# Kernel optimization log

Measured on AMD Instinct MI355X. Metric: run time of the kernel, lower is better.

## Reference

```python
import jax, jax.numpy as jnp
import numpy as np

N, F, T, C, E = 5000, 4, 12, 600, 160000


def setup_inputs() -> dict:
    key = jax.random.key(0)
    ks = jax.random.split(key, 18)
    x = jax.random.normal(ks[0], (N, F, T), jnp.float32)
    edge_index = jax.random.randint(ks[1], (2, E), 0, N)
    edge_attributes = jax.random.uniform(ks[2], (E,), jnp.float32)
    s_in = 0.5   # glorot-ish scale for F->C conv weights
    s_lin = 0.03  # scale for (2C)->C gate linears
    return {
        "x": x,
        "edge_index": edge_index,
        "edge_attributes": edge_attributes,
        # GCNConv weights/biases for z, r, h gates (weight stored [F, C])
        "W_z": jax.random.normal(ks[3], (F, C), jnp.float32) * s_in,
        "b_z": jnp.zeros((C,), jnp.float32),
        "W_r": jax.random.normal(ks[4], (F, C), jnp.float32) * s_in,
        "b_r": jnp.zeros((C,), jnp.float32),
        "W_h": jax.random.normal(ks[5], (F, C), jnp.float32) * s_in,
        "b_h": jnp.zeros((C,), jnp.float32),
        # gate Linear(2C, C) weights in torch layout [out=C, in=2C]
        "Wlz": jax.random.normal(ks[6], (C, 2 * C), jnp.float32) * s_lin,
        "blz": jnp.zeros((C,), jnp.float32),
        "Wlr": jax.random.normal(ks[7], (C, 2 * C), jnp.float32) * s_lin,
        "blr": jnp.zeros((C,), jnp.float32),
        "Wlh": jax.random.normal(ks[8], (C, 2 * C), jnp.float32) * s_lin,
        "blh": jnp.zeros((C,), jnp.float32),
        # temporal attention logits over periods
        "att": jax.random.normal(ks[9], (T,), jnp.float32),
        # head Linear(600, periods), torch layout [T, C]
        "W_head": jax.random.normal(ks[10], (T, C), jnp.float32) * 0.04,
        "b_head": jnp.zeros((T,), jnp.float32),
    }


def _gcn_propagate(x, edge_index, edge_weight):
    """A_hat @ x with A_hat = D^{-1/2}(A+I)D^{-1/2} (GCNConv norm, self-loops w=1).
    x: [N, F, T] -> [N, F, T]."""
    loop = jnp.arange(N)
    row = jnp.concatenate([edge_index[0], loop])   # source j
    col = jnp.concatenate([edge_index[1], loop])   # target i
    w = jnp.concatenate([edge_weight, jnp.ones((N,), x.dtype)])
    deg = jax.ops.segment_sum(w, col, num_segments=N)
    dis = jnp.where(deg > 0, jax.lax.rsqrt(deg), 0.0)
    norm = dis[row] * w * dis[col]                 # [E+N]
    msgs = norm[:, None, None] * x[row]            # gather + scale, [E+N, F, T]
    return jax.ops.segment_sum(msgs, col, num_segments=N)


def reference(x, edge_index, edge_attributes,
              W_z, b_z, W_r, b_r, W_h, b_h,
              Wlz, blz, Wlr, blr, Wlh, blh,
              att, W_head, b_head):
    # A3TGCN: H is passed as None each period -> zeros, never threaded across
    # time. Hence z*H == 0 and the H*r candidate term == 0 exactly; the r-gate
    # (W_r, b_r, Wlr, blr) and the second halves of Wlz/Wlh drop out of the math.
    agg = _gcn_propagate(x, edge_index, edge_attributes)          # [N, F, T]
    # GCNConv output = A_hat X W + b (linear commutes with propagation)
    conv_z = jnp.einsum('nft,fc->nct', agg, W_z) + b_z[:, None]   # [N, C, T]
    conv_h = jnp.einsum('nft,fc->nct', agg, W_h) + b_h[:, None]
    # gate linears on cat([conv, H]) with H = 0 -> only first C input columns
    z = jax.nn.sigmoid(jnp.einsum('nct,dc->ndt', conv_z, Wlz[:, :C]) + blz[:, None])
    h_tilde = jnp.tanh(jnp.einsum('nct,dc->ndt', conv_h, Wlh[:, :C]) + blh[:, None])
    H_t = (1.0 - z) * h_tilde                                      # z*H = 0
    probs = jax.nn.softmax(att)                                    # [T]
    H_accum = jnp.einsum('nct,t->nc', H_t, probs)                  # [N, C]
    return jax.nn.relu(H_accum) @ W_head.T + b_head                # [N, T]
```

## Files before the change

### kernel.cpp

```cpp
#include <hip/hip_runtime.h>

#define NN 5000
#define NF 4
#define NT 12
#define NC 600
#define NCP 640
#define NE 160000
#define FT 48
#define LOG2E 1.4426950408889634f

typedef float v2f __attribute__((ext_vector_type(2)));


__global__ void k_init(float* __restrict__ degcnt, float* __restrict__ tabG) {
    int i = blockIdx.x * blockDim.x + threadIdx.x;
    if (i < 10000) degcnt[i] = 0.f;
    else if (i < 24092) tabG[i - 10000] = 0.f;
}

#define CNT_BLOCKS 625
#define WB_WAVES 6132
__global__ __launch_bounds__(256) void k_count(
        const int* __restrict__ ei, const float* __restrict__ w,
        int* __restrict__ cnt, float* __restrict__ deg, int* __restrict__ rank,
        const float* __restrict__ Wz, const float* __restrict__ bz,
        const float* __restrict__ Wh, const float* __restrict__ bh,
        const float* __restrict__ Wlz, const float* __restrict__ blz,
        const float* __restrict__ Wlh, const float* __restrict__ blh,
        const float* __restrict__ att, const float* __restrict__ Whead,
        float* __restrict__ tabG) {
    int bid = blockIdx.x;
    int tid = threadIdx.x;
    if (bid < CNT_BLOCKS) {
        int e = bid * 256 + tid;
        if (e < NE) {
            int c = ei[NE + e];
            rank[e] = atomicAdd(&cnt[c], 1);
            atomicAdd(&deg[c], w[e]);
        }
        return;
    }
    int wid = (bid - CNT_BLOCKS) * 4 + (tid >> 6);
    int lane = tid & 63;
    if (wid >= WB_WAVES) return;

    if (wid < 6000) {
        const float* va;
        const float* vb;
        float scale, bias = 0.f;
        if (wid < 2400) {
            int f = wid / NC, d = wid % NC;
            va = Wz + f * NC; vb = Wlz + d * (2 * NC); scale = LOG2E;
        } else if (wid < 4800) {
            int j = wid - 2400;
            int f = j / NC, d = j % NC;
            va = Wh + f * NC; vb = Wlh + d * (2 * NC); scale = 2.0f * LOG2E;
        } else if (wid < 5400) {
            int d = wid - 4800;
            va = bz; vb = Wlz + d * (2 * NC); scale = LOG2E; bias = blz[d];
        } else {
            int d = wid - 5400;
            va = bh; vb = Wlh + d * (2 * NC); scale = 2.0f * LOG2E; bias = blh[d];
        }
        float s = 0.f;
        for (int c = lane; c < NC; c += 64) s = fmaf(va[c], vb[c], s);
#pragma unroll
        for (int off = 32; off > 0; off >>= 1) s += __shfl_down(s, off, 64);
        if (lane == 0) {
            float r = scale * (bias + s);
            if (wid < 2400) {
                int f = wid / NC, d = wid % NC;
                tabG[d * 4 + f] = r;
            } else if (wid < 4800) {
                int j = wid - 2400;
                int f = j / NC, d = j % NC;
                tabG[2560 + d * 4 + f] = r;
            } else if (wid < 5400) {
                tabG[5120 + (wid - 4800) * 2] = r;
            } else {
                tabG[5120 + (wid - 5400) * 2 + 1] = r;
            }
        }
    } else if (wid < 6012) {
        if (lane == 0) {
            int t = wid - 6000;
            float m = att[0];
            for (int k = 1; k < NT; ++k) m = fmaxf(m, att[k]);
            float ssum = 0.f;
            for (int k = 0; k < NT; ++k) ssum += __expf(att[k] - m);
            tabG[14080 + t] = __expf(att[t] - m) / ssum;
        }
    } else {
        int i = (wid - 6012) * 64 + lane;
        if (i < 7680) {
            int j = i & 3;
            int rest = i >> 2;
            int d = rest % NCP, q = rest / NCP;
            float v = (d < NC) ? Whead[(4 * q + j) * NC + d] : 0.f;
            tabG[6400 + i] = v;
        }
    }
}

#define SCAN_CHUNK 20
__global__ __launch_bounds__(256) void k_scan(const int* __restrict__ cnt,
                                              const float* __restrict__ deg,
                                              int* __restrict__ base,
                                              float* __restrict__ dis) {
    __shared__ int part[256];
    int t = threadIdx.x;
    int start = t * SCAN_CHUNK;
    int s = 0;
#pragma unroll
    for (int k = 0; k < SCAN_CHUNK; ++k) {
        int idx = start + k;
        if (idx < NN) s += cnt[idx];
    }
    part[t] = s;
    __syncthreads();
    for (int off = 1; off < 256; off <<= 1) {
        int v = (t >= off) ? part[t - off] : 0;
        __syncthreads();
        part[t] += v;
        __syncthreads();
    }
    int running = (t == 0) ? 0 : part[t - 1];
#pragma unroll
    for (int k = 0; k < SCAN_CHUNK; ++k) {
        int idx = start + k;
        if (idx < NN) {
            base[idx] = running;
            running += cnt[idx];
            dis[idx] = rsqrtf(1.0f + deg[idx]);
        }
    }
    if (t == 255) base[NN] = part[255];
}

__global__ void k_scatter(const int* __restrict__ ei, const float* __restrict__ w,
                          const float* __restrict__ dis,
                          const int* __restrict__ base, const int* __restrict__ rank,
                          int2* __restrict__ epak) {
    int e = blockIdx.x * blockDim.x + threadIdx.x;
    if (e < NE) {
        int r = ei[e];
        int c = ei[NE + e];
        float nu = dis[r] * w[e] * dis[c];
        int2 p; p.x = r; p.y = __float_as_int(nu);
        epak[base[c] + rank[e]] = p;
    }
}

__global__ __launch_bounds__(64) void k_gather(
        const float* __restrict__ x, const float* __restrict__ dis,
        const int2* __restrict__ epak, const int* __restrict__ base,
        float* __restrict__ agg) {
    int n = blockIdx.x;
    int lane = threadIdx.x;
    int b0 = base[n], b1 = base[n + 1];
    float dn = dis[n];
    float acc = 0.f;
    if (lane < FT) acc = dn * dn * x[n * FT + lane];
    int j = b0;
    for (; j + 3 < b1; j += 4) {
        int2 p0 = epak[j], p1 = epak[j + 1], p2 = epak[j + 2], p3 = epak[j + 3];
        float n0 = __int_as_float(p0.y);
        float n1 = __int_as_float(p1.y);
        float n2 = __int_as_float(p2.y);
        float n3 = __int_as_float(p3.y);
        if (lane < FT) {
            acc += n0 * x[p0.x * FT + lane];
            acc += n1 * x[p1.x * FT + lane];
            acc += n2 * x[p2.x * FT + lane];
            acc += n3 * x[p3.x * FT + lane];
        }
    }
    for (; j < b1; ++j) {
        int2 p0 = epak[j];
        float n0 = __int_as_float(p0.y);
        if (lane < FT) acc += n0 * x[p0.x * FT + lane];
    }
    if (lane < FT) agg[n * FT + lane] = acc;
}

__global__ __launch_bounds__(256) void k_main(
        const float* __restrict__ agg, const float* __restrict__ tabG,
        const float* __restrict__ bhead, float* __restrict__ out) {
    __shared__ float red[4][NT][16];
    int tid = threadIdx.x;
    int wid = __builtin_amdgcn_readfirstlane(tid >> 6);
    int lane = tid & 63;
    int n = blockIdx.x * 4 + wid;

    const float4* mz4 = (const float4*)tabG;
    const float4* mh4 = (const float4*)(tabG + 2560);
    const float2* bzh = (const float2*)(tabG + 5120);
    const float4* wt4 = (const float4*)(tabG + 6400);

    const v2f* ag2 = (const v2f*)(agg + n * FT);
    v2f A2[24];
#pragma unroll
    for (int i = 0; i < 24; ++i) A2[i] = ag2[i];

    v2f pp[6];
#pragma unroll
    for (int tp = 0; tp < 6; ++tp) { pp[tp].x = tabG[14080 + 2 * tp]; pp[tp].y = tabG[14080 + 2 * tp + 1]; }

    float outp[NT];
#pragma unroll
    for (int t = 0; t < NT; ++t) outp[t] = 0.f;

#pragma unroll
    for (int it = 0; it < 10; ++it) {
        int dd = it * 64 + lane;

        float4 mzv = mz4[dd];
        float4 mhv = mh4[dd];
        float2 bb = bzh[dd];

        v2f hacc; hacc.x = 0.f; hacc.y = 0.f;
#pragma unroll
        for (int tp = 0; tp < 6; ++tp) {
            v2f u; u.x = bb.x; u.y = bb.x;
            v2f v; v.x = bb.y; v.y = bb.y;
            u += A2[0 * 6 + tp] * mzv.x;
            u += A2[1 * 6 + tp] * mzv.y;
            u += A2[2 * 6 + tp] * mzv.z;
            u += A2[3 * 6 + tp] * mzv.w;
            v += A2[0 * 6 + tp] * mhv.x;
            v += A2[1 * 6 + tp] * mhv.y;
            v += A2[2 * 6 + tp] * mhv.z;
            v += A2[3 * 6 + tp] * mhv.w;
            v2f eu; eu.x = exp2f(u.x); eu.y = exp2f(u.y);
            v2f ev; ev.x = exp2f(v.x); ev.y = exp2f(v.y);
            v2f den = (eu + 1.f) * (ev + 1.f);
            v2f rd; rd.x = __builtin_amdgcn_rcpf(den.x); rd.y = __builtin_amdgcn_rcpf(den.y);
            v2f num = pp[tp] * (ev - 1.f);
            hacc += num * rd;
        }
        float r = fmaxf(hacc.x + hacc.y, 0.f);

        float4 w0 = wt4[0 * NCP + dd], w1 = wt4[1 * NCP + dd], w2 = wt4[2 * NCP + dd];
        outp[0]  = fmaf(r, w0.x, outp[0]);   outp[1]  = fmaf(r, w0.y, outp[1]);
        outp[2]  = fmaf(r, w0.z, outp[2]);   outp[3]  = fmaf(r, w0.w, outp[3]);
        outp[4]  = fmaf(r, w1.x, outp[4]);   outp[5]  = fmaf(r, w1.y, outp[5]);
        outp[6]  = fmaf(r, w1.z, outp[6]);   outp[7]  = fmaf(r, w1.w, outp[7]);
        outp[8]  = fmaf(r, w2.x, outp[8]);   outp[9]  = fmaf(r, w2.y, outp[9]);
        outp[10] = fmaf(r, w2.z, outp[10]);  outp[11] = fmaf(r, w2.w, outp[11]);
    }

#pragma unroll
    for (int t = 0; t < NT; ++t) {
        float v = outp[t];
        v += __shfl_xor(v, 32, 64);
        v += __shfl_xor(v, 16, 64);
        if (lane < 16) red[wid][t][lane] = v;
    }
    if (lane < NT) {
        const float4* row = (const float4*)red[wid][lane];
        float4 a = row[0], b = row[1], c = row[2], d = row[3];
        float s = ((a.x + a.y) + (a.z + a.w)) + ((b.x + b.y) + (b.z + b.w))
                + ((c.x + c.y) + (c.z + c.w)) + ((d.x + d.y) + (d.z + d.w));
        out[n * NT + lane] = s + bhead[lane];
    }
}

extern "C" void kernel_launch(void* const* d_in, const int* in_sizes, int n_in,
                              void* d_out, int out_size, void* d_ws, size_t ws_size,
                              hipStream_t stream) {
    const float* x     = (const float*)d_in[0];
    const int*   ei    = (const int*)d_in[1];
    const float* ea    = (const float*)d_in[2];
    const float* Wz    = (const float*)d_in[3];
    const float* bz    = (const float*)d_in[4];
    const float* Wh    = (const float*)d_in[7];
    const float* bh    = (const float*)d_in[8];
    const float* Wlz   = (const float*)d_in[9];
    const float* blz   = (const float*)d_in[10];
    const float* Wlh   = (const float*)d_in[13];
    const float* blh   = (const float*)d_in[14];
    const float* att   = (const float*)d_in[15];
    const float* Whead = (const float*)d_in[16];
    const float* bhead = (const float*)d_in[17];
    float* out = (float*)d_out;

    float* ws   = (float*)d_ws;
    float* deg  = ws;
    int*   cnt  = (int*)(ws + 5000);
    float* dis  = ws + 10000;
    int*   base = (int*)(ws + 15000);
    int*   rank = (int*)(ws + 20008);
    int2*  epak = (int2*)(ws + 180008);
    float* agg  = ws + 500008;
    float* tabG = ws + 740008;

    k_init<<<(24092 + 255) / 256, 256, 0, stream>>>(deg, tabG);
    k_count<<<CNT_BLOCKS + (WB_WAVES + 3) / 4, 256, 0, stream>>>(
        ei, ea, cnt, deg, rank,
        Wz, bz, Wh, bh, Wlz, blz, Wlh, blh, att, Whead, tabG);
    k_scan<<<1, 256, 0, stream>>>(cnt, deg, base, dis);
    k_scatter<<<(NE + 255) / 256, 256, 0, stream>>>(ei, ea, dis, base, rank, epak);
    k_gather<<<NN, 64, 0, stream>>>(x, dis, epak, base, agg);
    k_main<<<NN / 4, 256, 0, stream>>>(agg, tabG, bhead, out);
}
```

Baseline: 89.90 us.

## Compute degree from CSR segments instead of float atomics; apply normalization in gather

Removes the float atomicAdd for degree in the count kernel and instead sums edge weights per target node from the CSR-packed edges in a new per-node kernel. The scatter now stores raw edge weights, and the gather applies dis[source] per edge and dis[target] once at the end. It also adds an occupancy hint to k_main. This trades contended atomics for an extra kernel launch plus an extra random dis lookup per edge in the gather.

Measured after the change: 76.52 us. 1.17x faster.

```diff
diff --git a/kernel.cpp b/kernel.cpp
--- a/kernel.cpp
+++ b/kernel.cpp
@@ -12,17 +12,17 @@
 typedef float v2f __attribute__((ext_vector_type(2)));
 
 
-__global__ void k_init(float* __restrict__ degcnt, float* __restrict__ tabG) {
+__global__ void k_init(int* __restrict__ cnt, float* __restrict__ tabG) {
     int i = blockIdx.x * blockDim.x + threadIdx.x;
-    if (i < 10000) degcnt[i] = 0.f;
-    else if (i < 24092) tabG[i - 10000] = 0.f;
+    if (i < 5000) cnt[i] = 0;
+    else if (i < 19092) tabG[i - 5000] = 0.f;
 }
 
 #define CNT_BLOCKS 625
 #define WB_WAVES 6132
 __global__ __launch_bounds__(256) void k_count(
-        const int* __restrict__ ei, const float* __restrict__ w,
-        int* __restrict__ cnt, float* __restrict__ deg, int* __restrict__ rank,
+        const int* __restrict__ ei,
+        int* __restrict__ cnt, int* __restrict__ rank,
         const float* __restrict__ Wz, const float* __restrict__ bz,
         const float* __restrict__ Wh, const float* __restrict__ bh,
         const float* __restrict__ Wlz, const float* __restrict__ blz,
@@ -33,11 +33,7 @@
     int tid = threadIdx.x;
     if (bid < CNT_BLOCKS) {
         int e = bid * 256 + tid;
-        if (e < NE) {
-            int c = ei[NE + e];
-            rank[e] = atomicAdd(&cnt[c], 1);
-            atomicAdd(&deg[c], w[e]);
-        }
+        if (e < NE) rank[e] = atomicAdd(&cnt[ei[NE + e]], 1);
         return;
     }
     int wid = (bid - CNT_BLOCKS) * 4 + (tid >> 6);
@@ -104,9 +100,7 @@
 
 #define SCAN_CHUNK 20
 __global__ __launch_bounds__(256) void k_scan(const int* __restrict__ cnt,
-                                              const float* __restrict__ deg,
-                                              int* __restrict__ base,
-                                              float* __restrict__ dis) {
+                                              int* __restrict__ base) {
     __shared__ int part[256];
     int t = threadIdx.x;
     int start = t * SCAN_CHUNK;
@@ -131,24 +125,32 @@
         if (idx < NN) {
             base[idx] = running;
             running += cnt[idx];
-            dis[idx] = rsqrtf(1.0f + deg[idx]);
         }
     }
     if (t == 255) base[NN] = part[255];
 }
 
 __global__ void k_scatter(const int* __restrict__ ei, const float* __restrict__ w,
-                          const float* __restrict__ dis,
                           const int* __restrict__ base, const int* __restrict__ rank,
                           int2* __restrict__ epak) {
     int e = blockIdx.x * blockDim.x + threadIdx.x;
     if (e < NE) {
-        int r = ei[e];
-        int c = ei[NE + e];
-        float nu = dis[r] * w[e] * dis[c];
-        int2 p; p.x = r; p.y = __float_as_int(nu);
-        epak[base[c] + rank[e]] = p;
-    }
+        int2 p; p.x = ei[e]; p.y = __float_as_int(w[e]);
+        epak[base[ei[NE + e]] + rank[e]] = p;
+    }
+}
+
+__global__ __launch_bounds__(64) void k_deg_dis(const int2* __restrict__ epak,
+                                                const int* __restrict__ base,
+                                                float* __restrict__ dis) {
+    int n = blockIdx.x;
+    int lane = threadIdx.x;
+    int b0 = base[n], b1 = base[n + 1];
+    float s = 0.f;
+    for (int j = b0 + lane; j < b1; j += 64) s += __int_as_float(epak[j].y);
+#pragma unroll
+    for (int off = 32; off > 0; off >>= 1) s += __shfl_down(s, off, 64);
+    if (lane == 0) dis[n] = rsqrtf(1.0f + s);
 }
 
 __global__ __launch_bounds__(64) void k_gather(
@@ -160,14 +162,14 @@
     int b0 = base[n], b1 = base[n + 1];
     float dn = dis[n];
     float acc = 0.f;
-    if (lane < FT) acc = dn * dn * x[n * FT + lane];
+    if (lane < FT) acc = dn * x[n * FT + lane];
     int j = b0;
     for (; j + 3 < b1; j += 4) {
         int2 p0 = epak[j], p1 = epak[j + 1], p2 = epak[j + 2], p3 = epak[j + 3];
-        float n0 = __int_as_float(p0.y);
-        float n1 = __int_as_float(p1.y);
-        float n2 = __int_as_float(p2.y);
-        float n3 = __int_as_float(p3.y);
+        float n0 = dis[p0.x] * __int_as_float(p0.y);
+        float n1 = dis[p1.x] * __int_as_float(p1.y);
+        float n2 = dis[p2.x] * __int_as_float(p2.y);
+        float n3 = dis[p3.x] * __int_as_float(p3.y);
         if (lane < FT) {
             acc += n0 * x[p0.x * FT + lane];
             acc += n1 * x[p1.x * FT + lane];
@@ -177,13 +179,13 @@
     }
     for (; j < b1; ++j) {
         int2 p0 = epak[j];
-        float n0 = __int_as_float(p0.y);
+        float n0 = dis[p0.x] * __int_as_float(p0.y);
         if (lane < FT) acc += n0 * x[p0.x * FT + lane];
     }
-    if (lane < FT) agg[n * FT + lane] = acc;
-}
-
-__global__ __launch_bounds__(256) void k_main(
+    if (lane < FT) agg[n * FT + lane] = dn * acc;
+}
+
+__global__ __launch_bounds__(256, 4) void k_main(
         const float* __restrict__ agg, const float* __restrict__ tabG,
         const float* __restrict__ bhead, float* __restrict__ out) {
     __shared__ float red[4][NT][16];
@@ -285,21 +287,21 @@
     float* out = (float*)d_out;
 
     float* ws   = (float*)d_ws;
-    float* deg  = ws;
-    int*   cnt  = (int*)(ws + 5000);
-    float* dis  = ws + 10000;
-    int*   base = (int*)(ws + 15000);
-    int*   rank = (int*)(ws + 20008);
-    int2*  epak = (int2*)(ws + 180008);
-    float* agg  = ws + 500008;
-    float* tabG = ws + 740008;
-
-    k_init<<<(24092 + 255) / 256, 256, 0, stream>>>(deg, tabG);
+    int*   cnt  = (int*)ws;
+    int*   base = (int*)(ws + 5000);
+    int*   rank = (int*)(ws + 10008);
+    int2*  epak = (int2*)(ws + 170008);
+    float* dis  = ws + 490008;
+    float* agg  = ws + 495008;
+    float* tabG = ws + 735008;
+
+    k_init<<<(19092 + 255) / 256, 256, 0, stream>>>(cnt, tabG);
     k_count<<<CNT_BLOCKS + (WB_WAVES + 3) / 4, 256, 0, stream>>>(
-        ei, ea, cnt, deg, rank,
+        ei, cnt, rank,
         Wz, bz, Wh, bh, Wlz, blz, Wlh, blh, att, Whead, tabG);
-    k_scan<<<1, 256, 0, stream>>>(cnt, deg, base, dis);
-    k_scatter<<<(NE + 255) / 256, 256, 0, stream>>>(ei, ea, dis, base, rank, epak);
+    k_scan<<<1, 256, 0, stream>>>(cnt, base);
+    k_scatter<<<(NE + 255) / 256, 256, 0, stream>>>(ei, ea, base, rank, epak);
+    k_deg_dis<<<NN, 64, 0, stream>>>(epak, base, dis);
     k_gather<<<NN, 64, 0, stream>>>(x, dis, epak, base, agg);
     k_main<<<NN / 4, 256, 0, stream>>>(agg, tabG, bhead, out);
 }
```
